# Optimization experiments

Hardware: AMD Instinct MI355X
Metric: run time of the kernel (lower is better)

Reference implementation:

```python
import jax, jax.numpy as jnp
import numpy as np

S = 7          # side
B = 2          # boxes per cell
C = 20         # classes
L = S * S      # grid cells
NOOBJ = 0.5 * 1.0
OBJ   = 0.5 * 1.0
CLS   = 0.5 * 1.0
COORD = 0.5 * 5.0


def setup_inputs() -> dict:
    key = jax.random.key(0)
    k1, k2, k3 = jax.random.split(key, 3)
    n = 16384
    preds = jax.random.uniform(k1, (n, L * (C + 5 * B)), dtype=jnp.float32)
    labels = jax.random.uniform(k2, (n, L * (1 + C + 4)), dtype=jnp.float32)
    lab = labels.reshape(n, L, 1 + C + 4)
    obj_flag = (jax.random.uniform(k3, (n, L)) < 0.15).astype(jnp.float32)
    lab = lab.at[:, :, 0].set(obj_flag)
    labels = lab.reshape(n, -1)
    return {"preds": preds, "labels": labels}


def _iou(t, o):
    # t, o: [..., 4] boxes in (cx, cy, w, h); returns [...]
    left   = jnp.maximum(t[..., 0] - 0.5 * t[..., 2], o[..., 0] - 0.5 * o[..., 2])
    right  = jnp.minimum(t[..., 0] + 0.5 * t[..., 2], o[..., 0] + 0.5 * o[..., 2])
    top    = jnp.maximum(t[..., 1] - 0.5 * t[..., 3], o[..., 1] - 0.5 * o[..., 3])
    bottom = jnp.minimum(t[..., 1] + 0.5 * t[..., 3], o[..., 1] + 0.5 * o[..., 3])
    w = right - left
    h = bottom - top
    invalid = (w < 0) | (h < 0)
    inter = jnp.where(invalid, 0.0, w * h)
    union = t[..., 2] * t[..., 3] + o[..., 2] * o[..., 3] - inter
    return jnp.where(invalid, 0.0, inter / jnp.maximum(union, 1e-12))


def reference(preds, labels):
    n = preds.shape[0]
    pcls  = preds[:, : L * C].reshape(n, L, C)                       # [n,L,C]
    pconf = preds[:, L * C : L * C + L * B].reshape(n, L, B)          # [n,L,B]
    pbox  = preds[:, L * C + L * B :].reshape(n, L, B, 4)             # [n,L,B,4]

    lab  = labels.reshape(n, L, 1 + C + 4)
    obj  = lab[:, :, 0] != 0                                          # [n,L]
    tcls = lab[:, :, 1 : 1 + C]                                       # [n,L,C]
    tbox = lab[:, :, 1 + C :]                                         # [n,L,4] raw

    # --- best-box selection (on detached predictions, like .detach() in torch) ---
    o_raw = jax.lax.stop_gradient(pbox)
    o = jnp.concatenate([o_raw[..., :2] / S, o_raw[..., 2:] ** 2], axis=-1)      # [n,L,B,4]
    t = jnp.concatenate([tbox[..., :2] / S, tbox[..., 2:]], axis=-1)[:, :, None] # [n,L,1,4]
    t = jax.lax.stop_gradient(t)

    iou  = _iou(t, o)                                                 # [n,L,B]
    rmse = jnp.sqrt(jnp.sum((t - o) ** 2, axis=-1))                   # [n,L,B]
    max_iou = jnp.max(iou, axis=-1)
    # if any IoU>0 pick first argmax of IoU, else first argmin of RMSE (best_rmse init 20)
    best = jnp.where(max_iou > 0, jnp.argmax(iou, axis=-1), jnp.argmin(rmse, axis=-1))  # [n,L]
    best_iou = jnp.take_along_axis(iou, best[:, :, None], axis=-1)[..., 0]        # [n,L]

    onehot = jnp.arange(B) == best[:, :, None]                        # [n,L,B]
    mask_best = obj[:, :, None] & onehot

    # confidence delta: noobject everywhere, overwritten at best box of object cells
    conf_delta = jnp.where(mask_best,
                           OBJ * (best_iou[:, :, None] - pconf) ** 2,
                           NOOBJ * pconf ** 2)

    # class delta (object cells only)
    cls_delta = jnp.where(obj[:, :, None], CLS * (tcls - pcls) ** 2, 0.0)

    # coord delta at best box: raw truth x,y and sqrt(truth w,h) vs raw preds
    pbest = jnp.take_along_axis(pbox, best[:, :, None, None], axis=2)[:, :, 0]    # [n,L,4]
    ttarget = jnp.concatenate([tbox[..., :2], jnp.sqrt(tbox[..., 2:])], axis=-1)  # [n,L,4]
    coord_delta = jnp.where(obj[:, :, None], COORD * (ttarget - pbest) ** 2, 0.0)

    return jnp.nansum(conf_delta) + jnp.nansum(cls_delta) + jnp.nansum(coord_delta)
```

## Files before the change

### kernel.cpp

```cpp
#include <hip/hip_runtime.h>


#define L_CELLS 49
#define PRED_ROW 1470
#define LAB_ROW 1225
#define CONF_BASE 980
#define BOX_BASE 1078
#define W_NOOBJ 0.5f
#define W_OBJ 0.5f
#define W_CLS 0.5f
#define W_COORD 2.5f
#define INV_S (1.0f / 7.0f)

#define LAB_SLOTS 308
#define WAVE_SLOTS 310

typedef int __attribute__((address_space(1))) as1_int;
typedef int __attribute__((address_space(3))) as3_int;

__global__ __launch_bounds__(256, 5) void yolo_loss_kernel(
    const float* __restrict__ preds, const float* __restrict__ labels,
    float* __restrict__ ws) {
  __shared__ float4 st[4][WAVE_SLOTS];

  const int tid = threadIdx.x;
  const int w = tid >> 6;
  const int lane = tid & 63;
  const int s = blockIdx.x * 4 + w;
  float4* stw = st[w];

  size_t g0 = (size_t)s * LAB_ROW;
  size_t ga = g0 & ~(size_t)3;
  int loff = (int)(g0 - ga);
#pragma unroll
  for (int r = 0; r < 5; ++r) {
    int i = lane + 64 * r;
    if (i < LAB_SLOTS) {
      __builtin_amdgcn_global_load_lds(
          (const as1_int*)(labels + ga + 4 * (size_t)i),
          (as3_int*)((float*)stw + 256 * r), 16, 0, 0);
    }
  }

  const float* rp = preds + (size_t)s * PRED_ROW;

  float2 cf = make_float2(0.f, 0.f);
  float2 pc[10];
  float2 bq[4];
  if (lane < L_CELLS) {
    const int l = lane;
    cf = *(const float2*)(rp + CONF_BASE + 2 * l);
#pragma unroll
    for (int k = 0; k < 10; ++k)
      pc[k] = *(const float2*)(rp + 20 * l + 2 * k);
#pragma unroll
    for (int k = 0; k < 4; ++k)
      bq[k] = *(const float2*)(rp + BOX_BASE + 8 * l + 2 * k);
  }

  asm volatile("s_waitcnt vmcnt(0)" ::: "memory");
  __builtin_amdgcn_sched_barrier(0);

  const float* lab = (const float*)stw + loff;

  float acc = 0.0f;
  if (lane < L_CELLS) {
    const int l = lane;
    float c0v = cf.x, c1v = cf.y;
    float objf = lab[25 * l];

    float noobj_term = W_NOOBJ * (c0v * c0v + c1v * c1v);

    float bx[8] = {bq[0].x, bq[0].y, bq[1].x, bq[1].y,
                   bq[2].x, bq[2].y, bq[3].x, bq[3].y};
    float tx = lab[25 * l + 21], ty = lab[25 * l + 22];
    float tw = lab[25 * l + 23], th = lab[25 * l + 24];
    float t0 = tx * INV_S, t1 = ty * INV_S, t2 = tw, t3 = th;

    float iou[2], rmse2[2];
#pragma unroll
    for (int b = 0; b < 2; ++b) {
      float o0 = bx[4 * b + 0] * INV_S;
      float o1 = bx[4 * b + 1] * INV_S;
      float o2 = bx[4 * b + 2] * bx[4 * b + 2];
      float o3 = bx[4 * b + 3] * bx[4 * b + 3];
      float left = fmaxf(t0 - 0.5f * t2, o0 - 0.5f * o2);
      float right = fminf(t0 + 0.5f * t2, o0 + 0.5f * o2);
      float top = fmaxf(t1 - 0.5f * t3, o1 - 0.5f * o3);
      float bot = fminf(t1 + 0.5f * t3, o1 + 0.5f * o3);
      float wd = right - left;
      float h = bot - top;
      bool invalid = (wd < 0.0f) || (h < 0.0f);
      float inter = invalid ? 0.0f : wd * h;
      float uni = t2 * t3 + o2 * o3 - inter;
      iou[b] = invalid ? 0.0f : inter / fmaxf(uni, 1e-12f);
      float d0 = t0 - o0, d1 = t1 - o1, d2 = t2 - o2, d3 = t3 - o3;
      rmse2[b] = d0 * d0 + d1 * d1 + d2 * d2 + d3 * d3;
    }

    float max_iou = fmaxf(iou[0], iou[1]);
    int best;
    if (max_iou > 0.0f)
      best = (iou[1] > iou[0]) ? 1 : 0;
    else
      best = (rmse2[1] < rmse2[0]) ? 1 : 0;
    float best_iou = iou[best];

    float cb = (best == 0) ? c0v : c1v;
    float co = (best == 0) ? c1v : c0v;
    float db = best_iou - cb;
    float obj_term = W_OBJ * db * db + W_NOOBJ * co * co;

    float clsacc = 0.0f;
#pragma unroll
    for (int k = 0; k < 10; ++k) {
      float d0 = lab[25 * l + 1 + 2 * k] - pc[k].x;
      float d1 = lab[25 * l + 2 + 2 * k] - pc[k].y;
      clsacc += d0 * d0 + d1 * d1;
    }
    obj_term += W_CLS * clsacc;

    float e0 = tx - bx[best * 4 + 0];
    float e1 = ty - bx[best * 4 + 1];
    float e2 = sqrtf(tw) - bx[best * 4 + 2];
    float e3 = sqrtf(th) - bx[best * 4 + 3];
    obj_term += W_COORD * (e0 * e0 + e1 * e1 + e2 * e2 + e3 * e3);

    acc = (objf != 0.0f) ? obj_term : noobj_term;
  }

#pragma unroll
  for (int o = 32; o > 0; o >>= 1) acc += __shfl_down(acc, o);

  __shared__ float wsum[4];
  if (lane == 0) wsum[w] = acc;
  __syncthreads();
  if (tid == 0) ws[blockIdx.x] = wsum[0] + wsum[1] + wsum[2] + wsum[3];
}

__global__ __launch_bounds__(1024) void final_reduce_kernel(
    const float* __restrict__ ws, float* __restrict__ out, int m) {
  float acc = 0.0f;
  for (int i = threadIdx.x; i < m; i += 1024) acc += ws[i];
#pragma unroll
  for (int o = 32; o > 0; o >>= 1) acc += __shfl_down(acc, o);
  __shared__ float wsum[16];
  int wave = threadIdx.x >> 6;
  int lane = threadIdx.x & 63;
  if (lane == 0) wsum[wave] = acc;
  __syncthreads();
  if (threadIdx.x == 0) {
    float sum = 0.0f;
#pragma unroll
    for (int i = 0; i < 16; ++i) sum += wsum[i];
    out[0] = sum;
  }
}

extern "C" void kernel_launch(void* const* d_in, const int* in_sizes, int n_in,
                              void* d_out, int out_size, void* d_ws, size_t ws_size,
                              hipStream_t stream) {
  const float* preds = (const float*)d_in[0];
  const float* labels = (const float*)d_in[1];
  float* out = (float*)d_out;
  float* ws = (float*)d_ws;
  int n = in_sizes[0] / PRED_ROW;
  int blocks = n / 4;

  yolo_loss_kernel<<<blocks, 256, 0, stream>>>(preds, labels, ws);
  final_reduce_kernel<<<1, 1024, 0, stream>>>(ws, out, blocks);
}
```

Baseline: 190.2 us.

## Load class and box predictions only for object cells, gated on objectness flag

```diff
diff --git a/kernel.cpp b/kernel.cpp
--- a/kernel.cpp
+++ b/kernel.cpp
@@ -18,7 +18,7 @@
 typedef int __attribute__((address_space(1))) as1_int;
 typedef int __attribute__((address_space(3))) as3_int;
 
-__global__ __launch_bounds__(256, 5) void yolo_loss_kernel(
+__global__ __launch_bounds__(256, 6) void yolo_loss_kernel(
     const float* __restrict__ preds, const float* __restrict__ labels,
     float* __restrict__ ws) {
   __shared__ float4 st[4][WAVE_SLOTS];
@@ -28,6 +28,16 @@
   const int lane = tid & 63;
   const int s = blockIdx.x * 4 + w;
   float4* stw = st[w];
+  float* stf = (float*)stw;
+
+  const float* lrow = labels + (size_t)s * LAB_ROW;
+  const float* rp = preds + (size_t)s * PRED_ROW;
+  const bool act = lane < L_CELLS;
+
+  float objf = 0.0f;
+  if (act) objf = lrow[25 * lane];
+
+  float2 cf = *(const float2*)(rp + CONF_BASE + 2 * lane);
 
   size_t g0 = (size_t)s * LAB_ROW;
   size_t ga = g0 & ~(size_t)3;
@@ -35,98 +45,93 @@
 #pragma unroll
   for (int r = 0; r < 5; ++r) {
     int i = lane + 64 * r;
-    if (i < LAB_SLOTS) {
-      __builtin_amdgcn_global_load_lds(
-          (const as1_int*)(labels + ga + 4 * (size_t)i),
-          (as3_int*)((float*)stw + 256 * r), 16, 0, 0);
-    }
+    if (i < LAB_SLOTS)
+      __builtin_amdgcn_global_load_lds((const as1_int*)(labels + ga + 4 * (size_t)i),
+                                       (as3_int*)(stf + 256 * r), 16, 0, 0);
   }
+  __builtin_amdgcn_sched_barrier(0);
 
-  const float* rp = preds + (size_t)s * PRED_ROW;
-
-  float2 cf = make_float2(0.f, 0.f);
+  const bool objm = act && (objf != 0.0f);
   float2 pc[10];
   float2 bq[4];
-  if (lane < L_CELLS) {
-    const int l = lane;
-    cf = *(const float2*)(rp + CONF_BASE + 2 * l);
+  if (objm) {
 #pragma unroll
     for (int k = 0; k < 10; ++k)
-      pc[k] = *(const float2*)(rp + 20 * l + 2 * k);
+      pc[k] = *(const float2*)(rp + 20 * lane + 2 * k);
 #pragma unroll
     for (int k = 0; k < 4; ++k)
-      bq[k] = *(const float2*)(rp + BOX_BASE + 8 * l + 2 * k);
+      bq[k] = *(const float2*)(rp + BOX_BASE + 8 * lane + 2 * k);
   }
 
   asm volatile("s_waitcnt vmcnt(0)" ::: "memory");
   __builtin_amdgcn_sched_barrier(0);
 
-  const float* lab = (const float*)stw + loff;
+  const float* lab = stf + loff;
 
   float acc = 0.0f;
-  if (lane < L_CELLS) {
+  if (act) {
     const int l = lane;
-    float c0v = cf.x, c1v = cf.y;
-    float objf = lab[25 * l];
+    float noobj_term = W_NOOBJ * (cf.x * cf.x + cf.y * cf.y);
+    if (objm) {
+      float bx[8] = {bq[0].x, bq[0].y, bq[1].x, bq[1].y,
+                     bq[2].x, bq[2].y, bq[3].x, bq[3].y};
+      float tx = lab[25 * l + 21], ty = lab[25 * l + 22];
+      float tw = lab[25 * l + 23], th = lab[25 * l + 24];
+      float t0 = tx * INV_S, t1 = ty * INV_S, t2 = tw, t3 = th;
 
-    float noobj_term = W_NOOBJ * (c0v * c0v + c1v * c1v);
+      float iou[2], rmse2[2];
+#pragma unroll
+      for (int b = 0; b < 2; ++b) {
+        float o0 = bx[4 * b + 0] * INV_S;
+        float o1 = bx[4 * b + 1] * INV_S;
+        float o2 = bx[4 * b + 2] * bx[4 * b + 2];
+        float o3 = bx[4 * b + 3] * bx[4 * b + 3];
+        float left = fmaxf(t0 - 0.5f * t2, o0 - 0.5f * o2);
+        float right = fminf(t0 + 0.5f * t2, o0 + 0.5f * o2);
+        float top = fmaxf(t1 - 0.5f * t3, o1 - 0.5f * o3);
+        float bot = fminf(t1 + 0.5f * t3, o1 + 0.5f * o3);
+        float wd = right - left;
+        float h = bot - top;
+        bool invalid = (wd < 0.0f) || (h < 0.0f);
+        float inter = invalid ? 0.0f : wd * h;
+        float uni = t2 * t3 + o2 * o3 - inter;
+        iou[b] = invalid ? 0.0f : inter / fmaxf(uni, 1e-12f);
+        float d0 = t0 - o0, d1 = t1 - o1, d2 = t2 - o2, d3 = t3 - o3;
+        rmse2[b] = d0 * d0 + d1 * d1 + d2 * d2 + d3 * d3;
+      }
 
-    float bx[8] = {bq[0].x, bq[0].y, bq[1].x, bq[1].y,
-                   bq[2].x, bq[2].y, bq[3].x, bq[3].y};
-    float tx = lab[25 * l + 21], ty = lab[25 * l + 22];
-    float tw = lab[25 * l + 23], th = lab[25 * l + 24];
-    float t0 = tx * INV_S, t1 = ty * INV_S, t2 = tw, t3 = th;
+      float max_iou = fmaxf(iou[0], iou[1]);
+      int best;
+      if (max_iou > 0.0f)
+        best = (iou[1] > iou[0]) ? 1 : 0;
+      else
+        best = (rmse2[1] < rmse2[0]) ? 1 : 0;
+      float best_iou = iou[best];
 
-    float iou[2], rmse2[2];
+      float cb = (best == 0) ? cf.x : cf.y;
+      float co = (best == 0) ? cf.y : cf.x;
+      float db = best_iou - cb;
+      float obj_term = W_OBJ * db * db + W_NOOBJ * co * co;
+
+      float clsacc = 0.0f;
 #pragma unroll
-    for (int b = 0; b < 2; ++b) {
-      float o0 = bx[4 * b + 0] * INV_S;
-      float o1 = bx[4 * b + 1] * INV_S;
-      float o2 = bx[4 * b + 2] * bx[4 * b + 2];
-      float o3 = bx[4 * b + 3] * bx[4 * b + 3];
-      float left = fmaxf(t0 - 0.5f * t2, o0 - 0.5f * o2);
-      float right = fminf(t0 + 0.5f * t2, o0 + 0.5f * o2);
-      float top = fmaxf(t1 - 0.5f * t3, o1 - 0.5f * o3);
-      float bot = fminf(t1 + 0.5f * t3, o1 + 0.5f * o3);
-      float wd = right - left;
-      float h = bot - top;
-      bool invalid = (wd < 0.0f) || (h < 0.0f);
-      float inter = invalid ? 0.0f : wd * h;
-      float uni = t2 * t3 + o2 * o3 - inter;
-      iou[b] = invalid ? 0.0f : inter / fmaxf(uni, 1e-12f);
-      float d0 = t0 - o0, d1 = t1 - o1, d2 = t2 - o2, d3 = t3 - o3;
-      rmse2[b] = d0 * d0 + d1 * d1 + d2 * d2 + d3 * d3;
+      for (int k = 0; k < 10; ++k) {
+        float d0 = lab[25 * l + 1 + 2 * k] - pc[k].x;
+        float d1 = lab[25 * l + 2 + 2 * k] - pc[k].y;
+        clsacc += d0 * d0 + d1 * d1;
+      }
+      obj_term += W_CLS * clsacc;
+
+      float e0 = tx - bx[best * 4 + 0];
+      float e1 = ty - bx[best * 4 + 1];
+      float e2 = sqrtf(tw) - bx[best * 4 + 2];
+      float e3 = sqrtf(th) - bx[best * 4 + 3];
+      obj_term += W_COORD * (e0 * e0 + e1 * e1 + e2 * e2 + e3 * e3);
+
+      acc = obj_term;
+    } else {
+      acc = noobj_term;
     }
-
-    float max_iou = fmaxf(iou[0], iou[1]);
-    int best;
-    if (max_iou > 0.0f)
-      best = (iou[1] > iou[0]) ? 1 : 0;
-    else
-      best = (rmse2[1] < rmse2[0]) ? 1 : 0;
-    float best_iou = iou[best];
-
-    float cb = (best == 0) ? c0v : c1v;
-    float co = (best == 0) ? c1v : c0v;
-    float db = best_iou - cb;
-    float obj_term = W_OBJ * db * db + W_NOOBJ * co * co;
-
-    float clsacc = 0.0f;
-#pragma unroll
-    for (int k = 0; k < 10; ++k) {
-      float d0 = lab[25 * l + 1 + 2 * k] - pc[k].x;
-      float d1 = lab[25 * l + 2 + 2 * k] - pc[k].y;
-      clsacc += d0 * d0 + d1 * d1;
-    }
-    obj_term += W_CLS * clsacc;
-
-    float e0 = tx - bx[best * 4 + 0];
-    float e1 = ty - bx[best * 4 + 1];
-    float e2 = sqrtf(tw) - bx[best * 4 + 2];
-    float e3 = sqrtf(th) - bx[best * 4 + 3];
-    obj_term += W_COORD * (e0 * e0 + e1 * e1 + e2 * e2 + e3 * e3);
-
-    acc = (objf != 0.0f) ? obj_term : noobj_term;
   }
 
 #pragma unroll
```

After: 186.2 us. 2.1% less time.
